# Performance work log

Hardware: AMD Instinct MI355X
Metric: run time of the kernel (lower is better)

The kernel has to match this reference:

```python
import jax, jax.numpy as jnp
import numpy as np

N_QUBIT = 22
N_LAYERS = 2
D_LOGICAL = 2  # num_logical_dim (one logical qubit)
DIM = 2 ** N_QUBIT


def _apply_ry(psi, th, q):
    # psi: (B, 2^n) complex64; Ry(th) on qubit q (q=0 is the most significant bit)
    half = th * 0.5
    c = jnp.cos(half).astype(jnp.complex64)
    s = jnp.sin(half).astype(jnp.complex64)
    psi4 = psi.reshape(psi.shape[0], 2 ** q, 2, -1)
    p0, p1 = psi4[:, :, 0], psi4[:, :, 1]
    out = jnp.stack([c * p0 - s * p1, s * p0 + c * p1], axis=2)
    return out.reshape(psi.shape)


def _apply_cnot(psi, c, t):
    a, b = (c, t) if c < t else (t, c)
    right = 2 ** (N_QUBIT - b - 1)
    mid = 2 ** (b - a - 1)
    psi6 = psi.reshape(psi.shape[0], 2 ** a, 2, mid, 2, right)
    if c < t:
        # control is axis 2; flip target axis 4 where control==1
        psi6 = psi6.at[:, :, 1, :, :, :].set(psi6[:, :, 1, :, ::-1, :])
    else:
        # control is axis 4; flip target axis 2 where control==1
        psi6 = psi6.at[:, :, :, :, 1, :].set(psi6[:, :, ::-1, :, 1, :])
    return psi6.reshape(psi.shape)


def _apply_pauli(psi, p, q):
    psi4 = psi.reshape(psi.shape[0], 2 ** q, 2, -1)
    p0, p1 = psi4[:, :, 0], psi4[:, :, 1]
    if p == 'X':
        out = jnp.stack([p1, p0], axis=2)
    elif p == 'Y':
        out = jnp.stack([-1j * p1, 1j * p0], axis=2)
    else:  # Z
        out = jnp.stack([p0, -p1], axis=2)
    return out.reshape(psi.shape)


def _encode(theta):
    # q0[i, i] = 1 for the logical basis states, then run the circuit
    psi = jnp.zeros((D_LOGICAL, DIM), jnp.complex64)
    psi = psi.at[jnp.arange(D_LOGICAL), jnp.arange(D_LOGICAL)].set(1.0)
    for l in range(N_LAYERS):
        for q in range(N_QUBIT):
            psi = _apply_ry(psi, theta[l, q], q)
        for q in range(N_QUBIT):
            psi = _apply_cnot(psi, q, (q + 1) % N_QUBIT)
    return psi


def _kl_loss(theta):
    psi = _encode(theta)  # (D_LOGICAL, 2^n)
    # Knill-Laflamme inner products T_e[i,j] = <psi_i| E_e |psi_j> for all weight-1 Paulis
    Ts = []
    for q in range(N_QUBIT):
        for p in ('X', 'Y', 'Z'):
            epsi = _apply_pauli(psi, p, q)
            Ts.append(jnp.einsum('is,js->ij', psi.conj(), epsi))
    T = jnp.stack(Ts)  # (3*N_QUBIT, D_LOGICAL, D_LOGICAL)
    diag = jnp.diagonal(T, axis1=1, axis2=2)
    lam = diag.mean(axis=1)  # per-error lambda_e
    res = T - lam[:, None, None] * jnp.eye(D_LOGICAL, dtype=T.dtype)
    # loss_type == 'L2'
    return jnp.sum(jnp.abs(res) ** 2)


def setup_inputs() -> dict:
    key = jax.random.key(0)
    theta = jax.random.normal(key, (N_LAYERS, N_QUBIT), dtype=jnp.float32)
    return {"theta": theta}


def reference(theta):
    return _kl_loss(theta)
```

## Files before the change

kernel.cpp:

```cpp
#include <hip/hip_runtime.h>

#define NQ 22
#define DIMN (1u << NQ)

struct MaskSet {
    unsigned L[NQ];
    unsigned Linv[NQ];
    unsigned xm[NQ];
    unsigned zm[NQ];
    unsigned frowHi[5];
};

constexpr MaskSet buildMasks() {
    MaskSet M{};
    for (int b = 0; b < NQ; ++b) M.L[b] = 1u << b;
    for (int q = 0; q < NQ; ++q) {
        int bc = NQ - 1 - q, bt = NQ - 1 - ((q + 1) % NQ);
        M.L[bt] ^= M.L[bc];
    }
    unsigned mat[NQ] = {}, aug[NQ] = {};
    for (int b = 0; b < NQ; ++b) { mat[b] = M.L[b]; aug[b] = 1u << b; }
    for (int col = 0; col < NQ; ++col) {
        int piv = col;
        while (!((mat[piv] >> col) & 1u)) ++piv;
        unsigned tm = mat[piv]; mat[piv] = mat[col]; mat[col] = tm;
        unsigned ta = aug[piv]; aug[piv] = aug[col]; aug[col] = ta;
        for (int r = 0; r < NQ; ++r)
            if (r != col && ((mat[r] >> col) & 1u)) { mat[r] ^= mat[col]; aug[r] ^= aug[col]; }
    }
    for (int b = 0; b < NQ; ++b) M.Linv[b] = aug[b];
    for (int j = 0; j < NQ; ++j) {
        int b = NQ - 1 - j;
        unsigned xmv = 0;
        for (int r = 0; r < NQ; ++r)
            if ((aug[r] >> b) & 1u) xmv |= 1u << r;
        M.xm[j] = xmv;
        M.zm[j] = M.L[b];
    }
    for (int j = 0; j < 5; ++j) {
        unsigned f = 0;
        for (int r = 0; r < NQ; ++r)
            if ((aug[r] >> (17 + j)) & 1u) f |= 1u << r;
        M.frowHi[j] = f;
    }
    return M;
}
constexpr int topbit_c(unsigned v) { int b = 0; while (v >> (b + 1)) ++b; return b; }
constexpr unsigned unionHi() {
    MaskSet M = buildMasks();
    unsigned u = 0;
    for (int j = 0; j < 5; ++j) u |= M.frowHi[j];
    return u;
}
static_assert((unionHi() & 0xFFFFu) == 0, "frowHi must only touch bits 16..21");

constexpr unsigned orbGen(int which) {
    MaskSet M = buildMasks();
    return (which == 0 ? M.xm[0] : which == 1 ? M.xm[4] : M.xm[9]) >> 2;
}
constexpr int orbS21() {
    MaskSet M = buildMasks();
    unsigned GA = M.xm[0] >> 2, GB = M.xm[4] >> 2, GC = M.xm[9] >> 2;
    unsigned GQ = M.xm[21] >> 2;
    for (int s = 1; s < 8; ++s) {
        unsigned c = ((s & 1) ? GA : 0u) ^ ((s & 2) ? GB : 0u) ^ ((s & 4) ? GC : 0u);
        if (c == GQ) return s;
    }
    return -1;
}
constexpr bool orbitOK() {
    unsigned GA = orbGen(0), GB = orbGen(1), GC = orbGen(2);
    int cA = topbit_c(GA), cB = topbit_c(GB), cC = topbit_c(GC);
    if (!(cC < cB && cB < cA) || cA > 19) return false;
    if (((GA >> cB) & 1u) || ((GA >> cC) & 1u)) return false;
    if (((GB >> cA) & 1u) || ((GB >> cC) & 1u)) return false;
    if (((GC >> cA) & 1u) || ((GC >> cB) & 1u)) return false;
    return orbS21() > 0;
}
static_assert(orbitOK(), "orbit structure for fused slice measurement must hold");

__device__ __forceinline__ float fflip(float v, unsigned sbit31) {
    return __int_as_float(__float_as_int(v) ^ (int)sbit31);
}
__device__ __forceinline__ unsigned ph4(unsigned g) { return g ^ ((g >> 6) & 3u); }

__device__ __forceinline__ float fold4(float a, float b, float c, float d, int lane) {
    bool p0 = (lane & 1) != 0;
    float kL = p0 ? b : a, sL = p0 ? a : b;
    kL += __shfl_xor(sL, 1);
    float kH = p0 ? d : c, sH = p0 ? c : d;
    kH += __shfl_xor(sH, 1);
    bool p1 = (lane & 2) != 0;
    float k2 = p1 ? kH : kL, s2 = p1 ? kL : kH;
    k2 += __shfl_xor(s2, 2);
    k2 += __shfl_xor(k2, 4);
    k2 += __shfl_xor(k2, 8);
    k2 += __shfl_xor(k2, 16);
    k2 += __shfl_xor(k2, 32);
    return k2;
}

__global__ __launch_bounds__(256) void k_prep(const float* __restrict__ theta,
                                              float* __restrict__ acc,
                                              float* __restrict__ trig) {
    int t = threadIdx.x;
    acc[t] = 0.f;
    if (t < 2 * NQ) {
        int l = t / NQ, q = t % NQ, b = NQ - 1 - q;
        float h = 0.5f * theta[t];
        trig[l * 2 * NQ + b]      = cosf(h);
        trig[l * 2 * NQ + NQ + b] = sinf(h);
    }
}

__global__ __launch_bounds__(256, 1) void k_genHi(float* __restrict__ phi,
                                                  const float* __restrict__ trig,
                                                  float* __restrict__ acc) {
    constexpr MaskSet M = buildMasks();
    __shared__ float red[4 * 12];
    unsigned base = blockIdx.x * 256u + threadIdx.x;
    unsigned P0 = 0;
#pragma unroll
    for (int b = 0; b < NQ; ++b)
        P0 |= ((unsigned)__popc(base & M.Linv[b]) & 1u) << b;
    float pc = 1.f;
#pragma unroll
    for (int b = 1; b < 16; ++b) {
        float cvb = trig[b], svb = trig[NQ + b];
        pc *= ((P0 >> b) & 1u) ? svb : cvb;
    }
    float cv0 = trig[0], sv0 = trig[NQ];
    float C0 = pc * ((P0 & 1u) ? sv0 : cv0);
    float C1 = pc * ((P0 & 1u) ? cv0 : -sv0);
    float cb[6], sb[6];
#pragma unroll
    for (int k = 0; k < 6; ++k) { cb[k] = trig[16 + k]; sb[k] = trig[NQ + 16 + k]; }
    unsigned u0 = P0 >> 16;
    float v0[32], v1[32];
#pragma unroll
    for (int e = 0; e < 32; ++e) {
        unsigned F = 0;
        if (e & 1)  F ^= M.frowHi[0];
        if (e & 2)  F ^= M.frowHi[1];
        if (e & 4)  F ^= M.frowHi[2];
        if (e & 8)  F ^= M.frowHi[3];
        if (e & 16) F ^= M.frowHi[4];
        unsigned u = u0 ^ (F >> 16);
        float vp = (u & 1u) ? sb[0] : cb[0];
#pragma unroll
        for (int k = 1; k < 6; ++k) vp *= ((u >> k) & 1u) ? sb[k] : cb[k];
        v0[e] = vp * C0;
        v1[e] = vp * C1;
    }
    float c2[5], s2[5];
#pragma unroll
    for (int j = 0; j < 5; ++j) {
        c2[j] = trig[2 * NQ + 17 + j];
        s2[j] = trig[3 * NQ + 17 + j];
    }
#pragma unroll
    for (int j = 0; j < 5; ++j) {
#pragma unroll
        for (int e = 0; e < 32; ++e) {
            if (!(e & (1 << j))) {
                int e1 = e | (1 << j);
                float a0 = v0[e], a1 = v0[e1];
                v0[e]  = c2[j] * a0 - s2[j] * a1;
                v0[e1] = s2[j] * a0 + c2[j] * a1;
                float b0 = v1[e], b1 = v1[e1];
                v1[e]  = c2[j] * b0 - s2[j] * b1;
                v1[e1] = s2[j] * b0 + c2[j] * b1;
            }
        }
    }
#pragma unroll
    for (int e = 0; e < 32; ++e) {
        unsigned a = base | ((unsigned)e << 17);
        phi[a] = v0[e];
        phi[DIMN + a] = v1[e];
    }
    int lane = threadIdx.x & 63, w = threadIdx.x >> 6;
#pragma unroll
    for (int i = 1; i <= 3; ++i) {
        unsigned ex  = M.xm[i] >> 17;
        unsigned zme = M.zm[i] >> 17;
        float t00 = 0.f, t11 = 0.f, t01 = 0.f, u01 = 0.f;
#pragma unroll
        for (int e = 0; e < 32; ++e) {
            int ep = e ^ (int)ex;
            t00 += v0[e] * v0[ep];
            t11 += v1[e] * v1[ep];
            float p = v0[e] * v1[ep];
            t01 += p;
            unsigned sg = ((unsigned)__popc((unsigned)ep & zme) & 1u) << 31;
            u01 += fflip(p, sg);
        }
        float r = fold4(t00, t11, t01, u01, lane);
        if (lane < 4) red[w * 12 + (i - 1) * 4 + lane] = r;
    }
    __syncthreads();
    int t = threadIdx.x;
    if (t < 12) {
        float r = red[t] + red[12 + t] + red[24 + t] + red[36 + t];
        atomicAdd(&acc[4 + t], r);
    }
}

__global__ __launch_bounds__(256, 1) void k_midA(float* __restrict__ phi,
                                                 const float* __restrict__ trig,
                                                 float* __restrict__ acc) {
    constexpr MaskSet M = buildMasks();
    __shared__ float red[4 * 16];
    unsigned tid = blockIdx.x * 256u + threadIdx.x;
    unsigned base = (tid & 0xFFFu) | ((tid >> 12) << 17);
    float v0[32], v1[32];
#pragma unroll
    for (int e = 0; e < 32; ++e) {
        unsigned a = base | ((unsigned)e << 12);
        v0[e] = phi[a];
        v1[e] = phi[DIMN + a];
    }
    float c[5], s[5];
#pragma unroll
    for (int j = 0; j < 5; ++j) {
        c[j] = trig[2 * NQ + 12 + j];
        s[j] = trig[3 * NQ + 12 + j];
    }
#pragma unroll
    for (int j = 0; j < 5; ++j) {
#pragma unroll
        for (int e = 0; e < 32; ++e) {
            if (!(e & (1 << j))) {
                int e1 = e | (1 << j);
                float a0 = v0[e], a1 = v0[e1];
                v0[e]  = c[j] * a0 - s[j] * a1;
                v0[e1] = s[j] * a0 + c[j] * a1;
                float b0 = v1[e], b1 = v1[e1];
                v1[e]  = c[j] * b0 - s[j] * b1;
                v1[e1] = s[j] * b0 + c[j] * b1;
            }
        }
    }
#pragma unroll
    for (int e = 0; e < 32; ++e) {
        unsigned a = base | ((unsigned)e << 12);
        phi[a] = v0[e];
        phi[DIMN + a] = v1[e];
    }
    int lane = threadIdx.x & 63, w = threadIdx.x >> 6;
#pragma unroll
    for (int i = 5; i <= 8; ++i) {
        unsigned ex  = (M.xm[i] >> 12) & 31u;
        unsigned zme = (M.zm[i] >> 12) & 31u;
        unsigned bs31 = ((unsigned)__popc(base & M.zm[i]) & 1u) << 31;
        float t00 = 0.f, t11 = 0.f, t01 = 0.f, u01 = 0.f;
#pragma unroll
        for (int e = 0; e < 32; ++e) {
            int ep = e ^ (int)ex;
            t00 += v0[e] * v0[ep];
            t11 += v1[e] * v1[ep];
            float p = v0[e] * v1[ep];
            t01 += p;
            unsigned sg = ((unsigned)__popc((unsigned)ep & zme) & 1u) << 31;
            u01 += fflip(p, sg ^ bs31);
        }
        float r = fold4(t00, t11, t01, u01, lane);
        if (lane < 4) red[w * 16 + (i - 5) * 4 + lane] = r;
    }
    __syncthreads();
    int t = threadIdx.x;
    if (t < 16) {
        float r = red[t] + red[16 + t] + red[32 + t] + red[48 + t];
        atomicAdd(&acc[20 + t], r);
    }
}

__global__ __launch_bounds__(256) void k_low(float* __restrict__ phi,
                                             const float* __restrict__ trig,
                                             float* __restrict__ acc) {
    constexpr MaskSet M = buildMasks();
    __shared__ float As[4096];
    __shared__ float Bs[4096];
    __shared__ float red[4 * 44];
    float4* As4 = (float4*)As;
    float4* Bs4 = (float4*)Bs;
    int t = threadIdx.x;
    unsigned base = blockIdx.x * 4096u;
    float a[16], b[16];

    {
        const float4* g0 = (const float4*)(phi + base);
        const float4* g1 = (const float4*)(phi + DIMN + base);
#pragma unroll
        for (int k = 0; k < 4; ++k) {
            float4 va = g0[4 * t + k];
            a[4 * k] = va.x; a[4 * k + 1] = va.y; a[4 * k + 2] = va.z; a[4 * k + 3] = va.w;
            float4 vb = g1[4 * t + k];
            b[4 * k] = vb.x; b[4 * k + 1] = vb.y; b[4 * k + 2] = vb.z; b[4 * k + 3] = vb.w;
        }
#pragma unroll
        for (int g = 0; g < 4; ++g) {
            float c = trig[2 * NQ + g], s = trig[3 * NQ + g];
#pragma unroll
            for (int e = 0; e < 16; ++e) {
                if (!(e & (1 << g))) {
                    int e1 = e | (1 << g);
                    float x0 = a[e], x1 = a[e1];
                    a[e] = c * x0 - s * x1; a[e1] = s * x0 + c * x1;
                    float y0 = b[e], y1 = b[e1];
                    b[e] = c * y0 - s * y1; b[e1] = s * y0 + c * y1;
                }
            }
        }
        unsigned sw = (unsigned)(t >> 4) & 3u;
#pragma unroll
        for (int k = 0; k < 4; ++k) {
            unsigned f = ((unsigned)(4 * t + k)) ^ sw;
            As4[f] = make_float4(a[4 * k], a[4 * k + 1], a[4 * k + 2], a[4 * k + 3]);
            Bs4[f] = make_float4(b[4 * k], b[4 * k + 1], b[4 * k + 2], b[4 * k + 3]);
        }
    }
    __syncthreads();

    {
        unsigned lo = (unsigned)t & 15u, hi = (unsigned)t >> 4;
        unsigned swz = (hi & 3u) << 2;
#pragma unroll
        for (int j = 0; j < 16; ++j) {
            unsigned i = lo | ((unsigned)j << 4) | (hi << 8);
            a[j] = As[i ^ swz];
            b[j] = Bs[i ^ swz];
        }
#pragma unroll
        for (int g = 0; g < 4; ++g) {
            float c = trig[2 * NQ + 4 + g], s = trig[3 * NQ + 4 + g];
#pragma unroll
            for (int e = 0; e < 16; ++e) {
                if (!(e & (1 << g))) {
                    int e1 = e | (1 << g);
                    float x0 = a[e], x1 = a[e1];
                    a[e] = c * x0 - s * x1; a[e1] = s * x0 + c * x1;
                    float y0 = b[e], y1 = b[e1];
                    b[e] = c * y0 - s * y1; b[e1] = s * y0 + c * y1;
                }
            }
        }
#pragma unroll
        for (int j = 0; j < 16; ++j) {
            unsigned i = lo | ((unsigned)j << 4) | (hi << 8);
            As[i ^ swz] = a[j];
            Bs[i ^ swz] = b[j];
        }
    }
    __syncthreads();

    {
#pragma unroll
        for (int j = 0; j < 16; ++j) {
            unsigned i = (unsigned)t | ((unsigned)j << 8);
            unsigned p = i ^ (((unsigned)j & 3u) << 2);
            a[j] = As[p];
            b[j] = Bs[p];
        }
#pragma unroll
        for (int g = 0; g < 4; ++g) {
            float c = trig[2 * NQ + 8 + g], s = trig[3 * NQ + 8 + g];
#pragma unroll
            for (int e = 0; e < 16; ++e) {
                if (!(e & (1 << g))) {
                    int e1 = e | (1 << g);
                    float x0 = a[e], x1 = a[e1];
                    a[e] = c * x0 - s * x1; a[e1] = s * x0 + c * x1;
                    float y0 = b[e], y1 = b[e1];
                    b[e] = c * y0 - s * y1; b[e1] = s * y0 + c * y1;
                }
            }
        }
#pragma unroll
        for (int j = 0; j < 16; ++j) {
            unsigned i = (unsigned)t | ((unsigned)j << 8);
            phi[base + i] = a[j];
            phi[DIMN + base + i] = b[j];
            unsigned p = i ^ (((unsigned)j & 3u) << 2);
            As[p] = a[j];
            Bs[p] = b[j];
        }
    }

    float SSv[3], z0v[3], z1v[3], z2v[3], d4v[3];
    {
#pragma unroll
        for (int c = 0; c < 3; ++c) {
            float p[16];
#pragma unroll
            for (int j = 0; j < 16; ++j)
                p[j] = (c == 0) ? a[j] * a[j] : (c == 1) ? b[j] * b[j] : a[j] * b[j];
            float s1[8], d1[8];
#pragma unroll
            for (int j = 0; j < 8; ++j) { s1[j] = p[j] + p[j + 8]; d1[j] = p[j] - p[j + 8]; }
            float s2[4], d2[4];
#pragma unroll
            for (int j = 0; j < 4; ++j) { s2[j] = s1[j] + s1[j + 4]; d2[j] = d1[j] - d1[j + 4]; }
            float d3a = d2[0] - d2[2], d3b = d2[1] - d2[3];
            SSv[c] = (s2[0] + s2[1]) + (s2[2] + s2[3]);
            z0v[c] = ((d1[0] + d1[1]) + (d1[2] + d1[3])) + ((d1[4] + d1[5]) + (d1[6] + d1[7]));
            z1v[c] = (d2[0] + d2[1]) + (d2[2] + d2[3]);
            z2v[c] = d3a + d3b;
            d4v[c] = d3a - d3b;
        }
    }
    int lane = t & 63, w = t >> 6;
#pragma unroll
    for (int c = 0; c < 3; ++c) {
        float r = fold4(SSv[c], z0v[c], z1v[c], z2v[c], lane);
        if (lane < 4) red[w * 33 + c * 11 + lane] = r;
        float v = d4v[c];
#pragma unroll
        for (int s2 = 0; s2 < 6; ++s2) {
            float u = __shfl_xor(v, 1 << s2);
            v = u + fflip(v, ((unsigned)(lane >> s2) & 1u) << 31);
        }
        int pcnt = __popc(lane);
        if (lane == 64 - (64 >> pcnt)) red[w * 33 + c * 11 + 4 + pcnt] = v;
    }
    __syncthreads();
    if (t < 66) {
        int c = t % 3, q = t / 3;
        int idx, wm;
        if (q == 0 || q == 21)      { idx = 10;    wm = 3; }
        else if (q <= 9)            { idx = 0;     wm = 0; }
        else if (q <= 13)           { idx = q - 9; wm = 0; }
        else if (q == 14)           { idx = 4;     wm = 2; }
        else if (q == 15)           { idx = 4;     wm = 3; }
        else                        { idx = q - 11; wm = 3; }
        float val = 0.f;
#pragma unroll
        for (int ww = 0; ww < 4; ++ww) {
            float rv = red[ww * 33 + c * 11 + idx];
            val += ((__popc(ww & wm) & 1) ? -rv : rv);
        }
        unsigned sg = (unsigned)__popc(base & M.zm[q]) & 1u;
        atomicAdd(&acc[4 * NQ + 3 * q + c], sg ? -val : val);
    }
    __syncthreads();

#pragma unroll
    for (int i = 0; i < 3; ++i) {
        constexpr int qn0 = 10;
        unsigned je  = (M.xm[qn0 + i] >> 8) & 15u;
        unsigned zmj = (M.zm[qn0 + i] >> 8) & 15u;
        unsigned zb31 = ((unsigned)__popc(base & M.zm[qn0 + i]) & 1u) << 31;
        float t00 = 0.f, t11 = 0.f, t01 = 0.f, u01 = 0.f;
#pragma unroll
        for (int j = 0; j < 16; ++j) {
            int jp = j ^ (int)je;
            t00 += a[j] * a[jp];
            t11 += b[j] * b[jp];
            float p = a[j] * b[jp];
            t01 += p;
            unsigned sg = ((unsigned)__popc((unsigned)jp & zmj) & 1u) << 31;
            u01 += fflip(p, sg ^ zb31);
        }
        float r = fold4(t00, t11, t01, u01, lane);
        if (lane < 4) red[w * 44 + 4 * i + lane] = r;
    }

#pragma unroll
    for (int i = 3; i < 11; ++i) {
        unsigned m = M.xm[10 + i], zm = M.zm[10 + i];
        unsigned zb = (unsigned)__popc(base & zm) & 1u;
        float t00 = 0.f, t11 = 0.f, t01 = 0.f, u01 = 0.f;
        if (i < 10) {
            int gb = topbit_c(M.xm[10 + i]) - 2;
            unsigned mg4 = m >> 2;
            unsigned swap2 = m & 3u;
#pragma unroll
            for (int r = 0; r < 2; ++r) {
                unsigned gc = (unsigned)t + 256u * r;
                unsigned g = ((gc >> gb) << (gb + 1)) | (gc & ((1u << gb) - 1u));
                unsigned gx = g ^ mg4;
                float4 a0 = As4[ph4(g)],  a1 = Bs4[ph4(g)];
                float4 b0 = As4[ph4(gx)], b1 = Bs4[ph4(gx)];
                if (swap2) {
                    b0 = make_float4(b0.z, b0.w, b0.x, b0.y);
                    b1 = make_float4(b1.z, b1.w, b1.x, b1.y);
                }
                unsigned szg = ((unsigned)__popc((g << 2) & zm) + zb) & 1u;
                unsigned szx = ((unsigned)__popc((gx << 2) & zm) + zb) & 1u;
                unsigned fg = szg << 31, fx = szx << 31;
                const float* A0 = &a0.x; const float* A1 = &a1.x;
                const float* B0 = &b0.x; const float* B1 = &b1.x;
#pragma unroll
                for (int j = 0; j < 4; ++j) {
                    t00 += A0[j] * B0[j];
                    t11 += A1[j] * B1[j];
                    float p = A0[j] * B1[j], r2 = B0[j] * A1[j];
                    t01 += p + r2;
                    u01 += fflip(p, fx) + fflip(r2, fg);
                }
            }
            t00 *= 2.f; t11 *= 2.f;
        } else {
#pragma unroll
            for (int k = 0; k < 4; ++k) {
                unsigned g = (unsigned)t + 256u * k;
                float4 a0 = As4[ph4(g)], a1 = Bs4[ph4(g)];
                unsigned szg = ((unsigned)__popc((g << 2) & zm) + zb) & 1u;
                const float* A0 = &a0.x; const float* A1 = &a1.x;
#pragma unroll
                for (int j = 0; j < 4; ++j) {
                    int jx = j ^ 3;
                    float p = A0[j] * A0[jx];
                    float q2 = A1[j] * A1[jx];
                    float cr = A0[j] * A1[jx];
                    t00 += p; t11 += q2; t01 += cr;
                    unsigned sj = ((unsigned)(jx >> 1) & 1u) ^ szg;
                    u01 += fflip(cr, sj << 31);
                }
            }
        }
        float r = fold4(t00, t11, t01, u01, lane);
        if (lane < 4) red[w * 44 + 4 * i + lane] = r;
    }
    __syncthreads();
    if (t < 44) {
        float r = red[t] + red[44 + t] + red[88 + t] + red[132 + t];
        atomicAdd(&acc[40 + t], r);
    }
}

__global__ __launch_bounds__(256) void k_measF(const float* __restrict__ phi,
                                               float* __restrict__ acc) {
    constexpr MaskSet M = buildMasks();
    constexpr unsigned GA = orbGen(0), GB = orbGen(1), GC = orbGen(2);
    constexpr int pc0 = topbit_c(GC), pc1 = topbit_c(GB), pc2 = topbit_c(GA);
    __shared__ float red[4 * 16];
    unsigned t = blockIdx.x * 256u + threadIdx.x;
    unsigned g = t;
    g = ((g >> pc0) << (pc0 + 1)) | (g & ((1u << pc0) - 1u));
    g = ((g >> pc1) << (pc1 + 1)) | (g & ((1u << pc1) - 1u));
    g = ((g >> pc2) << (pc2 + 1)) | (g & ((1u << pc2) - 1u));
    const float4* P0 = (const float4*)phi;
    const float4* P1 = (const float4*)(phi + DIMN);
    unsigned idx[8];
    float4 u4[8], w4[8];
#pragma unroll
    for (int s = 0; s < 8; ++s) {
        idx[s] = g ^ ((s & 1) ? GA : 0u) ^ ((s & 2) ? GB : 0u) ^ ((s & 4) ? GC : 0u);
        u4[s] = P0[idx[s]];
        w4[s] = P1[idx[s]];
    }
    constexpr int QN[4] = { 0, 4, 9, 21 };
    constexpr int SX[4] = { 1, 2, 4, orbS21() };
    float res[16];
#pragma unroll
    for (int qi = 0; qi < 4; ++qi) {
        const unsigned xq = M.xm[QN[qi]];
        const unsigned zq = M.zm[QN[qi]];
        const int sx = SX[qi];
        const int mu = (int)(xq & 3u);
        const unsigned zh = zq >> 2, zl = zq & 3u;
        unsigned fz[8];
#pragma unroll
        for (int s = 0; s < 8; ++s)
            fz[s] = ((unsigned)__popc(idx[s] & zh) & 1u) << 31;
        unsigned pj31[4];
#pragma unroll
        for (int j = 0; j < 4; ++j)
            pj31[j] = ((unsigned)__popc((unsigned)j & zl) & 1u) << 31;
        float t00 = 0.f, t11 = 0.f, t01 = 0.f, u01 = 0.f;
#pragma unroll
        for (int s = 0; s < 8; ++s) {
            const int s2 = s ^ sx;
            const float* A0 = &u4[s].x;
            const float* A1 = &w4[s].x;
            const float* B0 = &u4[s2].x;
            const float* B1 = &w4[s2].x;
            const unsigned fe = fz[s2];
#pragma unroll
            for (int j = 0; j < 4; ++j) {
                const int jp = j ^ mu;
                t00 += A0[j] * B0[jp];
                t11 += A1[j] * B1[jp];
                float p = A0[j] * B1[jp];
                t01 += p;
                u01 += fflip(p, fe ^ pj31[jp]);
            }
        }
        res[4 * qi + 0] = t00; res[4 * qi + 1] = t11;
        res[4 * qi + 2] = t01; res[4 * qi + 3] = u01;
    }
    int lane = threadIdx.x & 63, w = threadIdx.x >> 6;
#pragma unroll
    for (int g4 = 0; g4 < 4; ++g4) {
        float r = fold4(res[4 * g4 + 0], res[4 * g4 + 1], res[4 * g4 + 2], res[4 * g4 + 3], lane);
        if (lane < 4) red[w * 16 + 4 * g4 + lane] = r;
    }
    __syncthreads();
    int tt = threadIdx.x;
    if (tt < 16) {
        int qi = tt >> 2;
        int base4 = (qi == 0) ? 0 : (qi == 1) ? 16 : (qi == 2) ? 36 : 84;
        float r = red[tt] + red[16 + tt] + red[32 + tt] + red[48 + tt];
        atomicAdd(&acc[base4 + (tt & 3)], r);
    }
}

__global__ __launch_bounds__(64) void k_final(const float* __restrict__ acc,
                                              float* __restrict__ out) {
    int t = threadIdx.x;
    float v = 0.f;
    if (t < NQ) {
        float t00 = acc[4 * t], t11 = acc[4 * t + 1];
        float t01 = acc[4 * t + 2], u01 = acc[4 * t + 3];
        float d = t00 - t11;
        v = 0.5f * d * d + 2.f * t01 * t01 + 2.f * u01 * u01;
    } else if (t < 2 * NQ) {
        int q = t - NQ;
        float z0 = acc[4 * NQ + 3 * q], z1 = acc[4 * NQ + 3 * q + 1];
        float zz = acc[4 * NQ + 3 * q + 2];
        float d = z0 - z1;
        v = 0.5f * d * d + 2.f * zz * zz;
    }
    v += __shfl_down(v, 32); v += __shfl_down(v, 16); v += __shfl_down(v, 8);
    v += __shfl_down(v, 4);  v += __shfl_down(v, 2);  v += __shfl_down(v, 1);
    if (t == 0) out[0] = v;
}

extern "C" void kernel_launch(void* const* d_in, const int* in_sizes, int n_in,
                              void* d_out, int out_size, void* d_ws, size_t ws_size,
                              hipStream_t stream) {
    const float* theta = (const float*)d_in[0];
    float* out  = (float*)d_out;
    float* ws   = (float*)d_ws;
    float* phi  = ws;
    float* acc  = ws + 2 * (size_t)DIMN;
    float* trig = acc + 256;

    k_prep<<<1, 256, 0, stream>>>(theta, acc, trig);
    k_genHi<<<512, 256, 0, stream>>>(phi, trig, acc);
    k_midA<<<512, 256, 0, stream>>>(phi, trig, acc);
    k_low<<<1024, 256, 0, stream>>>(phi, trig, acc);
    k_measF<<<512, 256, 0, stream>>>(phi, acc);
    k_final<<<1, 64, 0, stream>>>(acc, out);
}
```

Measured before the change: 157.7 us.

## Restructure k_low to 512 threads with 8-element radix-8 gate passes

k_low now uses 512 threads per block, each holding 8 amplitudes instead of 16, and applies the low 12 Ry gates in four 3-qubit passes through a new XOR-swizzled shared layout instead of three 4-qubit passes. The measurement stage is remapped to match: per-wave Z-parity reductions over 8 waves, a new qubit-to-index table, and a single pass per qubit for the paired measurements. The goal is more waves in flight with fewer registers per thread to hide shared-memory and global latency. The cost is an extra shared-memory round trip and barrier, plus a larger cross-wave reduction.

After: 156.3 us (median of 2 runs). About the same (-0.9%).

```diff
diff --git a/kernel.cpp b/kernel.cpp
--- a/kernel.cpp
+++ b/kernel.cpp
@@ -79,10 +79,29 @@
 }
 static_assert(orbitOK(), "orbit structure for fused slice measurement must hold");
 
+constexpr bool lowPlanOK() {
+    MaskSet M = buildMasks();
+    if ((M.xm[10] & ~0xE00u) != 0) return false;
+    if ((M.xm[11] & ~0xE00u) != 0) return false;
+    for (int q = 12; q <= 19; ++q) {
+        if ((M.xm[q] & 3u) != 0 && (M.xm[q] & 3u) != 2u) return false;
+        if ((M.zm[q] & 3u) != 0) return false;
+        if (topbit_c(M.xm[q]) < 2 || topbit_c(M.xm[q]) > 9) return false;
+    }
+    if (M.xm[20] != 3u) return false;
+    if ((M.zm[20] & 3u) != 2u) return false;
+    return true;
+}
+static_assert(lowPlanOK(), "k_low measurement plan must hold");
+
 __device__ __forceinline__ float fflip(float v, unsigned sbit31) {
     return __int_as_float(__float_as_int(v) ^ (int)sbit31);
 }
 __device__ __forceinline__ unsigned ph4(unsigned g) { return g ^ ((g >> 6) & 3u); }
+
+__device__ __forceinline__ unsigned sA(unsigned i) {
+    return i ^ ((i >> 3) & 7u) ^ (((i >> 6) & 3u) << 3);
+}
 
 __device__ __forceinline__ float fold4(float a, float b, float c, float d, int lane) {
     bool p0 = (lane & 1) != 0;
@@ -100,6 +119,23 @@
     return k2;
 }
 
+__device__ __forceinline__ void gates3(float* a, float* b, const float* __restrict__ trig, int b0) {
+#pragma unroll
+    for (int g = 0; g < 3; ++g) {
+        float c = trig[2 * NQ + b0 + g], s = trig[3 * NQ + b0 + g];
+#pragma unroll
+        for (int e = 0; e < 8; ++e) {
+            if (!(e & (1 << g))) {
+                int e1 = e | (1 << g);
+                float x0 = a[e], x1 = a[e1];
+                a[e] = c * x0 - s * x1; a[e1] = s * x0 + c * x1;
+                float y0 = b[e], y1 = b[e1];
+                b[e] = c * y0 - s * y1; b[e1] = s * y0 + c * y1;
+            }
+        }
+    }
+}
+
 __global__ __launch_bounds__(256) void k_prep(const float* __restrict__ theta,
                                               float* __restrict__ acc,
                                               float* __restrict__ trig) {
@@ -275,184 +311,154 @@
     }
 }
 
-__global__ __launch_bounds__(256) void k_low(float* __restrict__ phi,
-                                             const float* __restrict__ trig,
-                                             float* __restrict__ acc) {
+__global__ __launch_bounds__(512, 8) void k_low(float* __restrict__ phi,
+                                                const float* __restrict__ trig,
+                                                float* __restrict__ acc) {
     constexpr MaskSet M = buildMasks();
     __shared__ float As[4096];
     __shared__ float Bs[4096];
-    __shared__ float red[4 * 44];
+    __shared__ float redZ[8 * 33];
+    __shared__ float redQ[8 * 44];
     float4* As4 = (float4*)As;
     float4* Bs4 = (float4*)Bs;
     int t = threadIdx.x;
+    int lane = t & 63, w = t >> 6;
     unsigned base = blockIdx.x * 4096u;
-    float a[16], b[16];
+    float a[8], b[8];
 
     {
         const float4* g0 = (const float4*)(phi + base);
         const float4* g1 = (const float4*)(phi + DIMN + base);
 #pragma unroll
-        for (int k = 0; k < 4; ++k) {
-            float4 va = g0[4 * t + k];
+        for (int k = 0; k < 2; ++k) {
+            float4 va = g0[2 * t + k];
             a[4 * k] = va.x; a[4 * k + 1] = va.y; a[4 * k + 2] = va.z; a[4 * k + 3] = va.w;
-            float4 vb = g1[4 * t + k];
+            float4 vb = g1[2 * t + k];
             b[4 * k] = vb.x; b[4 * k + 1] = vb.y; b[4 * k + 2] = vb.z; b[4 * k + 3] = vb.w;
         }
-#pragma unroll
-        for (int g = 0; g < 4; ++g) {
-            float c = trig[2 * NQ + g], s = trig[3 * NQ + g];
-#pragma unroll
-            for (int e = 0; e < 16; ++e) {
-                if (!(e & (1 << g))) {
-                    int e1 = e | (1 << g);
-                    float x0 = a[e], x1 = a[e1];
-                    a[e] = c * x0 - s * x1; a[e1] = s * x0 + c * x1;
-                    float y0 = b[e], y1 = b[e1];
-                    b[e] = c * y0 - s * y1; b[e1] = s * y0 + c * y1;
-                }
-            }
-        }
-        unsigned sw = (unsigned)(t >> 4) & 3u;
-#pragma unroll
-        for (int k = 0; k < 4; ++k) {
-            unsigned f = ((unsigned)(4 * t + k)) ^ sw;
-            As4[f] = make_float4(a[4 * k], a[4 * k + 1], a[4 * k + 2], a[4 * k + 3]);
-            Bs4[f] = make_float4(b[4 * k], b[4 * k + 1], b[4 * k + 2], b[4 * k + 3]);
+        gates3(a, b, trig, 0);
+#pragma unroll
+        for (int j = 0; j < 8; ++j) {
+            unsigned i = ((unsigned)t << 3) | (unsigned)j;
+            unsigned A = sA(i);
+            As[A] = a[j]; Bs[A] = b[j];
         }
     }
     __syncthreads();
 
     {
-        unsigned lo = (unsigned)t & 15u, hi = (unsigned)t >> 4;
-        unsigned swz = (hi & 3u) << 2;
-#pragma unroll
-        for (int j = 0; j < 16; ++j) {
-            unsigned i = lo | ((unsigned)j << 4) | (hi << 8);
-            a[j] = As[i ^ swz];
-            b[j] = Bs[i ^ swz];
-        }
-#pragma unroll
-        for (int g = 0; g < 4; ++g) {
-            float c = trig[2 * NQ + 4 + g], s = trig[3 * NQ + 4 + g];
-#pragma unroll
-            for (int e = 0; e < 16; ++e) {
-                if (!(e & (1 << g))) {
-                    int e1 = e | (1 << g);
-                    float x0 = a[e], x1 = a[e1];
-                    a[e] = c * x0 - s * x1; a[e1] = s * x0 + c * x1;
-                    float y0 = b[e], y1 = b[e1];
-                    b[e] = c * y0 - s * y1; b[e1] = s * y0 + c * y1;
-                }
-            }
-        }
-#pragma unroll
-        for (int j = 0; j < 16; ++j) {
-            unsigned i = lo | ((unsigned)j << 4) | (hi << 8);
-            As[i ^ swz] = a[j];
-            Bs[i ^ swz] = b[j];
+#pragma unroll
+        for (int j = 0; j < 8; ++j) {
+            unsigned i = (((unsigned)t >> 3) << 6) | ((unsigned)j << 3) | ((unsigned)t & 7u);
+            unsigned A = sA(i);
+            a[j] = As[A]; b[j] = Bs[A];
+        }
+        gates3(a, b, trig, 3);
+#pragma unroll
+        for (int j = 0; j < 8; ++j) {
+            unsigned i = (((unsigned)t >> 3) << 6) | ((unsigned)j << 3) | ((unsigned)t & 7u);
+            unsigned A = sA(i);
+            As[A] = a[j]; Bs[A] = b[j];
         }
     }
     __syncthreads();
 
     {
 #pragma unroll
-        for (int j = 0; j < 16; ++j) {
-            unsigned i = (unsigned)t | ((unsigned)j << 8);
-            unsigned p = i ^ (((unsigned)j & 3u) << 2);
-            a[j] = As[p];
-            b[j] = Bs[p];
-        }
-#pragma unroll
-        for (int g = 0; g < 4; ++g) {
-            float c = trig[2 * NQ + 8 + g], s = trig[3 * NQ + 8 + g];
-#pragma unroll
-            for (int e = 0; e < 16; ++e) {
-                if (!(e & (1 << g))) {
-                    int e1 = e | (1 << g);
-                    float x0 = a[e], x1 = a[e1];
-                    a[e] = c * x0 - s * x1; a[e1] = s * x0 + c * x1;
-                    float y0 = b[e], y1 = b[e1];
-                    b[e] = c * y0 - s * y1; b[e1] = s * y0 + c * y1;
-                }
-            }
-        }
-#pragma unroll
-        for (int j = 0; j < 16; ++j) {
-            unsigned i = (unsigned)t | ((unsigned)j << 8);
-            phi[base + i] = a[j];
-            phi[DIMN + base + i] = b[j];
-            unsigned p = i ^ (((unsigned)j & 3u) << 2);
-            As[p] = a[j];
-            Bs[p] = b[j];
-        }
-    }
-
-    float SSv[3], z0v[3], z1v[3], z2v[3], d4v[3];
+        for (int j = 0; j < 8; ++j) {
+            unsigned i = (((unsigned)t >> 6) << 9) | ((unsigned)j << 6) | ((unsigned)t & 63u);
+            unsigned A = sA(i);
+            a[j] = As[A]; b[j] = Bs[A];
+        }
+        gates3(a, b, trig, 6);
+#pragma unroll
+        for (int j = 0; j < 8; ++j) {
+            unsigned i = (((unsigned)t >> 6) << 9) | ((unsigned)j << 6) | ((unsigned)t & 63u);
+            unsigned A = sA(i);
+            As[A] = a[j]; Bs[A] = b[j];
+        }
+    }
+    __syncthreads();
+
     {
 #pragma unroll
-        for (int c = 0; c < 3; ++c) {
-            float p[16];
-#pragma unroll
-            for (int j = 0; j < 16; ++j)
-                p[j] = (c == 0) ? a[j] * a[j] : (c == 1) ? b[j] * b[j] : a[j] * b[j];
-            float s1[8], d1[8];
-#pragma unroll
-            for (int j = 0; j < 8; ++j) { s1[j] = p[j] + p[j + 8]; d1[j] = p[j] - p[j + 8]; }
-            float s2[4], d2[4];
-#pragma unroll
-            for (int j = 0; j < 4; ++j) { s2[j] = s1[j] + s1[j + 4]; d2[j] = d1[j] - d1[j + 4]; }
-            float d3a = d2[0] - d2[2], d3b = d2[1] - d2[3];
-            SSv[c] = (s2[0] + s2[1]) + (s2[2] + s2[3]);
-            z0v[c] = ((d1[0] + d1[1]) + (d1[2] + d1[3])) + ((d1[4] + d1[5]) + (d1[6] + d1[7]));
-            z1v[c] = (d2[0] + d2[1]) + (d2[2] + d2[3]);
-            z2v[c] = d3a + d3b;
-            d4v[c] = d3a - d3b;
-        }
-    }
-    int lane = t & 63, w = t >> 6;
+        for (int j = 0; j < 8; ++j) {
+            unsigned i = ((unsigned)j << 9) | (unsigned)t;
+            unsigned A = sA(i);
+            a[j] = As[A]; b[j] = Bs[A];
+        }
+        gates3(a, b, trig, 9);
+    }
+    __syncthreads();
+
+#pragma unroll
+    for (int j = 0; j < 8; ++j) {
+        unsigned i = ((unsigned)j << 9) | (unsigned)t;
+        phi[base + i] = a[j];
+        phi[DIMN + base + i] = b[j];
+        unsigned p = i ^ (((i >> 8) & 3u) << 2);
+        As[p] = a[j]; Bs[p] = b[j];
+    }
+
 #pragma unroll
     for (int c = 0; c < 3; ++c) {
-        float r = fold4(SSv[c], z0v[c], z1v[c], z2v[c], lane);
-        if (lane < 4) red[w * 33 + c * 11 + lane] = r;
-        float v = d4v[c];
-#pragma unroll
-        for (int s2 = 0; s2 < 6; ++s2) {
-            float u = __shfl_xor(v, 1 << s2);
-            v = u + fflip(v, ((unsigned)(lane >> s2) & 1u) << 31);
+        float p[8];
+#pragma unroll
+        for (int j = 0; j < 8; ++j)
+            p[j] = (c == 0) ? a[j] * a[j] : (c == 1) ? b[j] * b[j] : a[j] * b[j];
+        float s1[4], d1[4];
+#pragma unroll
+        for (int j = 0; j < 4; ++j) { s1[j] = p[j] + p[j + 4]; d1[j] = p[j] - p[j + 4]; }
+        float s2_0 = s1[0] + s1[2], s2_1 = s1[1] + s1[3];
+        float d2_0 = d1[0] - d1[2], d2_1 = d1[1] - d1[3];
+        float SS = s2_0 + s2_1;
+        float z0 = (d1[0] + d1[1]) + (d1[2] + d1[3]);
+        float z1 = d2_0 + d2_1;
+        float d3 = d2_0 - d2_1;
+        float r = fold4(SS, z0, z1, 0.f, lane);
+        if (lane < 3) redZ[w * 33 + c * 11 + lane] = r;
+        float v = d3;
+#pragma unroll
+        for (int s = 0; s < 6; ++s) {
+            float u = __shfl_xor(v, 1 << s);
+            v = u + fflip(v, ((unsigned)(lane >> s) & 1u) << 31);
         }
         int pcnt = __popc(lane);
-        if (lane == 64 - (64 >> pcnt)) red[w * 33 + c * 11 + 4 + pcnt] = v;
-    }
-    __syncthreads();
+        if (lane == 64 - (64 >> pcnt)) redZ[w * 33 + c * 11 + 3 + pcnt] = v;
+    }
+    __syncthreads();
+
     if (t < 66) {
         int c = t % 3, q = t / 3;
         int idx, wm;
-        if (q == 0 || q == 21)      { idx = 10;    wm = 3; }
-        else if (q <= 9)            { idx = 0;     wm = 0; }
-        else if (q <= 13)           { idx = q - 9; wm = 0; }
-        else if (q == 14)           { idx = 4;     wm = 2; }
-        else if (q == 15)           { idx = 4;     wm = 3; }
-        else                        { idx = q - 11; wm = 3; }
+        if (q == 0 || q == 21)      { idx = 9; wm = 7; }
+        else if (q <= 9)            { idx = 0; wm = 0; }
+        else if (q == 10)           { idx = 1; wm = 0; }
+        else if (q == 11)           { idx = 2; wm = 0; }
+        else if (q == 12)           { idx = 3; wm = 0; }
+        else if (q == 13)           { idx = 3; wm = 4; }
+        else if (q == 14)           { idx = 3; wm = 6; }
+        else if (q == 15)           { idx = 3; wm = 7; }
+        else                        { idx = q - 12; wm = 7; }
         float val = 0.f;
 #pragma unroll
-        for (int ww = 0; ww < 4; ++ww) {
-            float rv = red[ww * 33 + c * 11 + idx];
+        for (int ww = 0; ww < 8; ++ww) {
+            float rv = redZ[ww * 33 + c * 11 + idx];
             val += ((__popc(ww & wm) & 1) ? -rv : rv);
         }
         unsigned sg = (unsigned)__popc(base & M.zm[q]) & 1u;
         atomicAdd(&acc[4 * NQ + 3 * q + c], sg ? -val : val);
     }
-    __syncthreads();
-
-#pragma unroll
-    for (int i = 0; i < 3; ++i) {
-        constexpr int qn0 = 10;
-        unsigned je  = (M.xm[qn0 + i] >> 8) & 15u;
-        unsigned zmj = (M.zm[qn0 + i] >> 8) & 15u;
-        unsigned zb31 = ((unsigned)__popc(base & M.zm[qn0 + i]) & 1u) << 31;
+
+#pragma unroll
+    for (int i = 0; i < 2; ++i) {
+        int q = 10 + i;
+        unsigned je  = (M.xm[q] >> 9) & 7u;
+        unsigned zmj = (M.zm[q] >> 9) & 7u;
+        unsigned zb31 = ((unsigned)__popc(base & M.zm[q]) & 1u) << 31;
         float t00 = 0.f, t11 = 0.f, t01 = 0.f, u01 = 0.f;
 #pragma unroll
-        for (int j = 0; j < 16; ++j) {
+        for (int j = 0; j < 8; ++j) {
             int jp = j ^ (int)je;
             t00 += a[j] * a[jp];
             t11 += b[j] * b[jp];
@@ -462,69 +468,73 @@
             u01 += fflip(p, sg ^ zb31);
         }
         float r = fold4(t00, t11, t01, u01, lane);
-        if (lane < 4) red[w * 44 + 4 * i + lane] = r;
-    }
-
-#pragma unroll
-    for (int i = 3; i < 11; ++i) {
-        unsigned m = M.xm[10 + i], zm = M.zm[10 + i];
+        if (lane < 4) redQ[w * 44 + 4 * i + lane] = r;
+    }
+
+#pragma unroll
+    for (int iq = 2; iq < 10; ++iq) {
+        int q = 10 + iq;
+        unsigned m = M.xm[q], zm = M.zm[q];
+        unsigned zb = (unsigned)__popc(base & zm) & 1u;
+        int gb = topbit_c(M.xm[q]) - 2;
+        unsigned mg4 = m >> 2;
+        unsigned swap2 = m & 3u;
+        float t00 = 0.f, t11 = 0.f, t01 = 0.f, u01 = 0.f;
+        unsigned gc = (unsigned)t;
+        unsigned g = ((gc >> gb) << (gb + 1)) | (gc & ((1u << gb) - 1u));
+        unsigned gx = g ^ mg4;
+        float4 a0 = As4[ph4(g)],  a1 = Bs4[ph4(g)];
+        float4 b0 = As4[ph4(gx)], b1 = Bs4[ph4(gx)];
+        if (swap2) {
+            b0 = make_float4(b0.z, b0.w, b0.x, b0.y);
+            b1 = make_float4(b1.z, b1.w, b1.x, b1.y);
+        }
+        unsigned szg = ((unsigned)__popc((g << 2) & zm) + zb) & 1u;
+        unsigned szx = ((unsigned)__popc((gx << 2) & zm) + zb) & 1u;
+        unsigned fg = szg << 31, fx = szx << 31;
+        const float* A0 = &a0.x; const float* A1 = &a1.x;
+        const float* B0 = &b0.x; const float* B1 = &b1.x;
+#pragma unroll
+        for (int j = 0; j < 4; ++j) {
+            t00 += A0[j] * B0[j];
+            t11 += A1[j] * B1[j];
+            float p = A0[j] * B1[j], r2 = B0[j] * A1[j];
+            t01 += p + r2;
+            u01 += fflip(p, fx) + fflip(r2, fg);
+        }
+        t00 *= 2.f; t11 *= 2.f;
+        float r = fold4(t00, t11, t01, u01, lane);
+        if (lane < 4) redQ[w * 44 + 4 * iq + lane] = r;
+    }
+    {
+        unsigned zm = M.zm[20];
         unsigned zb = (unsigned)__popc(base & zm) & 1u;
         float t00 = 0.f, t11 = 0.f, t01 = 0.f, u01 = 0.f;
-        if (i < 10) {
-            int gb = topbit_c(M.xm[10 + i]) - 2;
-            unsigned mg4 = m >> 2;
-            unsigned swap2 = m & 3u;
-#pragma unroll
-            for (int r = 0; r < 2; ++r) {
-                unsigned gc = (unsigned)t + 256u * r;
-                unsigned g = ((gc >> gb) << (gb + 1)) | (gc & ((1u << gb) - 1u));
-                unsigned gx = g ^ mg4;
-                float4 a0 = As4[ph4(g)],  a1 = Bs4[ph4(g)];
-                float4 b0 = As4[ph4(gx)], b1 = Bs4[ph4(gx)];
-                if (swap2) {
-                    b0 = make_float4(b0.z, b0.w, b0.x, b0.y);
-                    b1 = make_float4(b1.z, b1.w, b1.x, b1.y);
-                }
-                unsigned szg = ((unsigned)__popc((g << 2) & zm) + zb) & 1u;
-                unsigned szx = ((unsigned)__popc((gx << 2) & zm) + zb) & 1u;
-                unsigned fg = szg << 31, fx = szx << 31;
-                const float* A0 = &a0.x; const float* A1 = &a1.x;
-                const float* B0 = &b0.x; const float* B1 = &b1.x;
-#pragma unroll
-                for (int j = 0; j < 4; ++j) {
-                    t00 += A0[j] * B0[j];
-                    t11 += A1[j] * B1[j];
-                    float p = A0[j] * B1[j], r2 = B0[j] * A1[j];
-                    t01 += p + r2;
-                    u01 += fflip(p, fx) + fflip(r2, fg);
-                }
+#pragma unroll
+        for (int k = 0; k < 2; ++k) {
+            unsigned g = (unsigned)t + 512u * k;
+            float4 a0 = As4[ph4(g)], a1 = Bs4[ph4(g)];
+            unsigned szg = ((unsigned)__popc((g << 2) & zm) + zb) & 1u;
+            const float* A0 = &a0.x; const float* A1 = &a1.x;
+#pragma unroll
+            for (int j = 0; j < 4; ++j) {
+                int jx = j ^ 3;
+                float p = A0[j] * A0[jx];
+                float q2 = A1[j] * A1[jx];
+                float cr = A0[j] * A1[jx];
+                t00 += p; t11 += q2; t01 += cr;
+                unsigned sj = ((unsigned)(jx >> 1) & 1u) ^ szg;
+                u01 += fflip(cr, sj << 31);
             }
-            t00 *= 2.f; t11 *= 2.f;
-        } else {
-#pragma unroll
-            for (int k = 0; k < 4; ++k) {
-                unsigned g = (unsigned)t + 256u * k;
-                float4 a0 = As4[ph4(g)], a1 = Bs4[ph4(g)];
-                unsigned szg = ((unsigned)__popc((g << 2) & zm) + zb) & 1u;
-                const float* A0 = &a0.x; const float* A1 = &a1.x;
-#pragma unroll
-                for (int j = 0; j < 4; ++j) {
-                    int jx = j ^ 3;
-                    float p = A0[j] * A0[jx];
-                    float q2 = A1[j] * A1[jx];
-                    float cr = A0[j] * A1[jx];
-                    t00 += p; t11 += q2; t01 += cr;
-                    unsigned sj = ((unsigned)(jx >> 1) & 1u) ^ szg;
-                    u01 += fflip(cr, sj << 31);
-                }
-            }
         }
         float r = fold4(t00, t11, t01, u01, lane);
-        if (lane < 4) red[w * 44 + 4 * i + lane] = r;
+        if (lane < 4) redQ[w * 44 + 40 + lane] = r;
     }
     __syncthreads();
     if (t < 44) {
-        float r = red[t] + red[44 + t] + red[88 + t] + red[132 + t];
+        float r = 0.f;
+#pragma unroll
+        for (int ww = 0; ww < 8; ++ww) r += redQ[ww * 44 + t];
         atomicAdd(&acc[40 + t], r);
     }
 }
@@ -640,7 +650,7 @@
     k_prep<<<1, 256, 0, stream>>>(theta, acc, trig);
     k_genHi<<<512, 256, 0, stream>>>(phi, trig, acc);
     k_midA<<<512, 256, 0, stream>>>(phi, trig, acc);
-    k_low<<<1024, 256, 0, stream>>>(phi, trig, acc);
+    k_low<<<1024, 512, 0, stream>>>(phi, trig, acc);
     k_measF<<<512, 256, 0, stream>>>(phi, acc);
     k_final<<<1, 64, 0, stream>>>(acc, out);
 }
```
